# Kernel tuning notes

Measured on AMD Instinct MI355X. Metric: run time of the kernel, lower is better.

Reference implementation:

```python
import jax, jax.numpy as jnp
import numpy as np

B, M, K, N = 2, 4096, 4096, 4096

def setup_inputs() -> dict:
    key = jax.random.key(0)
    k1, k2 = jax.random.split(key)
    x = jax.random.normal(k1, (B, M, K), dtype=jnp.float32)
    y = jax.random.normal(k2, (B, N, K), dtype=jnp.float32)
    # set_activation_scale: clip = 2 * mean(|t|) when unset
    x_clip = (2.0 * jnp.abs(x).mean()).astype(jnp.float32)
    y_clip = (2.0 * jnp.abs(y).mean()).astype(jnp.float32)
    return {"x": x, "y": y, "x_clip": x_clip, "y_clip": y_clip}

def reference(x, y, x_clip, y_clip):
    # CUTLASS binary (XNOR/popcount) GEMM == sign(x) @ sign(y)^T, scaled by clips.
    # x: [B,M,K], y: [B,N,K] -> out: [B,M,N]
    out = jnp.einsum('bmk,bnk->bmn', jnp.sign(x), jnp.sign(y))
    return out * x_clip * y_clip
```

## Files before the change

### kernel.cpp

```cpp
#include <hip/hip_runtime.h>
#include <stdint.h>

#define B_ 2
#define M_ 4096
#define N_ 4096
#define K_ 4096
#define WPR 128
#define NCH 64
#define TM 128
#define TN 128
#define LDR 80

typedef int v4i  __attribute__((ext_vector_type(4)));
typedef int v16i __attribute__((ext_vector_type(16)));

__global__ __launch_bounds__(256) void pack_rows(
    const float* __restrict__ x, const float* __restrict__ y,
    uint32_t* __restrict__ px, uint32_t* __restrict__ py,
    int* __restrict__ rpx, int* __restrict__ rpy) {
    const float* in = blockIdx.y ? y : x;
    uint32_t* out   = blockIdx.y ? py : px;
    int* rp         = blockIdx.y ? rpy : rpx;
    const int wid  = (blockIdx.x * blockDim.x + threadIdx.x) >> 6;
    const int half = (threadIdx.x >> 5) & 1;
    const int l    = threadIdx.x & 31;
    const int row  = wid * 2 + half;
    const float4* src = (const float4*)(in + (size_t)row * K_);
    uint32_t r0 = 0, r1 = 0, r2 = 0, r3 = 0;
#pragma unroll 8
    for (int j = 0; j < 32; ++j) {
        float4 f = src[j * 32 + l];
        r0 = (r0 << 1) | (__float_as_uint(f.x) >> 31);
        r1 = (r1 << 1) | (__float_as_uint(f.y) >> 31);
        r2 = (r2 << 1) | (__float_as_uint(f.z) >> 31);
        r3 = (r3 << 1) | (__float_as_uint(f.w) >> 31);
    }
    ((uint4*)(out + (size_t)row * WPR))[l] = make_uint4(r0, r1, r2, r3);
    int p = __popc(r0) + __popc(r1) + __popc(r2) + __popc(r3);
#pragma unroll
    for (int off = 1; off < 32; off <<= 1) p += __shfl_xor(p, off);
    if (l == 0) rp[row] = p;
}

__global__ __launch_bounds__(256, 4) void bgemm_i8(
    const uint32_t* __restrict__ pxw, const uint32_t* __restrict__ pyw,
    const int* __restrict__ rpx, const int* __restrict__ rpy,
    float* __restrict__ out, const float* __restrict__ xclip,
    const float* __restrict__ yclip) {
    __shared__ uint8_t As[2][TM * LDR];
    __shared__ uint8_t Bs[2][TN * LDR];

    const int b    = blockIdx.z;
    const int m0   = blockIdx.x * TM;
    const int n0   = blockIdx.y * TN;
    const int t    = threadIdx.x;
    const int lane = t & 63;
    const int w    = t >> 6;
    const int wr   = w >> 1, wc = w & 1;

    const int er = t >> 1;
    const int wh = t & 1;
    const uint32_t* gA = pxw + ((size_t)(b * M_ + m0 + er)) * WPR + wh;
    const uint32_t* gB = pyw + ((size_t)(b * N_ + n0 + er)) * WPR + wh;

    v16i acc[2][2];
#pragma unroll
    for (int ti = 0; ti < 2; ++ti)
#pragma unroll
        for (int tj = 0; tj < 2; ++tj)
#pragma unroll
            for (int r = 0; r < 16; ++r) acc[ti][tj][r] = 0;

#define EXPAND_STORE(wv, base)                                              \
    {                                                                       \
        uint32_t d0 = (wv)&0x01010101u, d1 = ((wv) >> 1) & 0x01010101u;     \
        uint32_t d2 = ((wv) >> 2) & 0x01010101u, d3 = ((wv) >> 3) & 0x01010101u; \
        uint32_t d4 = ((wv) >> 4) & 0x01010101u, d5 = ((wv) >> 5) & 0x01010101u; \
        uint32_t d6 = ((wv) >> 6) & 0x01010101u, d7 = ((wv) >> 7) & 0x01010101u; \
        uint4* p_ = (uint4*)((base) + er * LDR + wh * 32);                  \
        p_[0] = make_uint4(d0, d1, d2, d3);                                 \
        p_[1] = make_uint4(d4, d5, d6, d7);                                 \
    }

    uint32_t wa = gA[0], wb = gB[0];
    EXPAND_STORE(wa, As[0]);
    EXPAND_STORE(wb, Bs[0]);
    __syncthreads();

    for (int c = 0; c < NCH; ++c) {
        const int buf = c & 1;
        if (c + 1 < NCH) {
            wa = gA[2 * (c + 1)];
            wb = gB[2 * (c + 1)];
        }
#pragma unroll
        for (int ks = 0; ks < 2; ++ks) {
            v4i af[2], bf[2];
#pragma unroll
            for (int ti = 0; ti < 2; ++ti) {
                int r = wr * 64 + ti * 32 + (lane & 31);
                af[ti] = *(const v4i*)(&As[buf][r * LDR + ks * 32 + (lane >> 5) * 16]);
            }
#pragma unroll
            for (int tj = 0; tj < 2; ++tj) {
                int r = wc * 64 + tj * 32 + (lane & 31);
                bf[tj] = *(const v4i*)(&Bs[buf][r * LDR + ks * 32 + (lane >> 5) * 16]);
            }
#pragma unroll
            for (int ti = 0; ti < 2; ++ti)
#pragma unroll
                for (int tj = 0; tj < 2; ++tj)
                    acc[ti][tj] = __builtin_amdgcn_mfma_i32_32x32x32_i8(
                        af[ti], bf[tj], acc[ti][tj], 0, 0, 0);
        }
        if (c + 1 < NCH) {
            EXPAND_STORE(wa, As[buf ^ 1]);
            EXPAND_STORE(wb, Bs[buf ^ 1]);
        }
        __syncthreads();
    }

    const float scale = xclip[0] * yclip[0];
    const int col   = lane & 31;
    const int rquad = (lane >> 5) * 4;
#pragma unroll
    for (int ti = 0; ti < 2; ++ti) {
#pragma unroll
        for (int r = 0; r < 16; ++r) {
            int rowl = (r & 3) + 8 * (r >> 2) + rquad;
            int mm = m0 + wr * 64 + ti * 32 + rowl;
            int pav = rpx[b * M_ + mm];
            float* orow = out + ((size_t)b * M_ + mm) * (size_t)N_;
#pragma unroll
            for (int tj = 0; tj < 2; ++tj) {
                int nn = n0 + wc * 64 + tj * 32 + col;
                int pbv = rpy[b * N_ + nn];
                int ci = K_ - 2 * (pav + pbv) + 4 * acc[ti][tj][r];
                orow[nn] = scale * (float)ci;
            }
        }
    }
}

extern "C" void kernel_launch(void* const* d_in, const int* in_sizes, int n_in,
                              void* d_out, int out_size, void* d_ws, size_t ws_size,
                              hipStream_t stream) {
    const float* x     = (const float*)d_in[0];
    const float* y     = (const float*)d_in[1];
    const float* xclip = (const float*)d_in[2];
    const float* yclip = (const float*)d_in[3];
    float* out = (float*)d_out;

    uint32_t* px = (uint32_t*)d_ws;
    uint32_t* py = px + (size_t)B_ * M_ * WPR;
    int* rpx = (int*)(py + (size_t)B_ * N_ * WPR);
    int* rpy = rpx + B_ * M_;

    hipLaunchKernelGGL(pack_rows, dim3(1024, 2), dim3(256), 0, stream,
                       x, y, px, py, rpx, rpy);

    dim3 grid(M_ / TM, N_ / TN, B_);
    hipLaunchKernelGGL(bgemm_i8, grid, dim3(256), 0, stream,
                       px, py, rpx, rpy, out, xclip, yclip);
}
```

Before: 440.2 us.

## Encode signs as FP4 ±1 and use scaled f8f6f4 MFMA

Each packed sign bit is expanded into an FP4 (E2M1) nibble encoding +1 or -1 instead of a 0/1 int8 byte. The GEMM then uses the MFMA 32x32x64 f8f6f4 scaled instruction in FP4 mode with unit scales, which doubles K per instruction and halves the main-loop trip count. Because ±1 values are multiplied directly, the popcount row sums and the K-2(pa+pb)+4acc correction are removed, so the pack kernel and epilogue get lighter. The risks are the correctness of the FP4 nibble layout and the fp32 accumulation, which is exact here because sums are bounded by K.

Measured after the change: 374.8 us. 1.17x faster.

```diff
diff --git a/kernel.cpp b/kernel.cpp
--- a/kernel.cpp
+++ b/kernel.cpp
@@ -6,21 +6,20 @@
 #define N_ 4096
 #define K_ 4096
 #define WPR 128
-#define NCH 64
+#define NIT 32
 #define TM 128
 #define TN 128
 #define LDR 80
 
-typedef int v4i  __attribute__((ext_vector_type(4)));
-typedef int v16i __attribute__((ext_vector_type(16)));
+typedef int v4i   __attribute__((ext_vector_type(4)));
+typedef int v8i   __attribute__((ext_vector_type(8)));
+typedef float v16f __attribute__((ext_vector_type(16)));
 
 __global__ __launch_bounds__(256) void pack_rows(
     const float* __restrict__ x, const float* __restrict__ y,
-    uint32_t* __restrict__ px, uint32_t* __restrict__ py,
-    int* __restrict__ rpx, int* __restrict__ rpy) {
+    uint32_t* __restrict__ px, uint32_t* __restrict__ py) {
     const float* in = blockIdx.y ? y : x;
     uint32_t* out   = blockIdx.y ? py : px;
-    int* rp         = blockIdx.y ? rpy : rpx;
     const int wid  = (blockIdx.x * blockDim.x + threadIdx.x) >> 6;
     const int half = (threadIdx.x >> 5) & 1;
     const int l    = threadIdx.x & 31;
@@ -36,15 +35,10 @@
         r3 = (r3 << 1) | (__float_as_uint(f.w) >> 31);
     }
     ((uint4*)(out + (size_t)row * WPR))[l] = make_uint4(r0, r1, r2, r3);
-    int p = __popc(r0) + __popc(r1) + __popc(r2) + __popc(r3);
-#pragma unroll
-    for (int off = 1; off < 32; off <<= 1) p += __shfl_xor(p, off);
-    if (l == 0) rp[row] = p;
 }
 
-__global__ __launch_bounds__(256, 4) void bgemm_i8(
+__global__ __launch_bounds__(256, 4) void bgemm_fp4(
     const uint32_t* __restrict__ pxw, const uint32_t* __restrict__ pyw,
-    const int* __restrict__ rpx, const int* __restrict__ rpy,
     float* __restrict__ out, const float* __restrict__ xclip,
     const float* __restrict__ yclip) {
     __shared__ uint8_t As[2][TM * LDR];
@@ -60,60 +54,71 @@
 
     const int er = t >> 1;
     const int wh = t & 1;
-    const uint32_t* gA = pxw + ((size_t)(b * M_ + m0 + er)) * WPR + wh;
-    const uint32_t* gB = pyw + ((size_t)(b * N_ + n0 + er)) * WPR + wh;
+    const uint32_t* gA = pxw + ((size_t)(b * M_ + m0 + er)) * WPR + 2 * wh;
+    const uint32_t* gB = pyw + ((size_t)(b * N_ + n0 + er)) * WPR + 2 * wh;
 
-    v16i acc[2][2];
+    v16f acc[2][2];
 #pragma unroll
     for (int ti = 0; ti < 2; ++ti)
 #pragma unroll
         for (int tj = 0; tj < 2; ++tj)
 #pragma unroll
-            for (int r = 0; r < 16; ++r) acc[ti][tj][r] = 0;
+            for (int r = 0; r < 16; ++r) acc[ti][tj][r] = 0.0f;
 
-#define EXPAND_STORE(wv, base)                                              \
-    {                                                                       \
-        uint32_t d0 = (wv)&0x01010101u, d1 = ((wv) >> 1) & 0x01010101u;     \
-        uint32_t d2 = ((wv) >> 2) & 0x01010101u, d3 = ((wv) >> 3) & 0x01010101u; \
-        uint32_t d4 = ((wv) >> 4) & 0x01010101u, d5 = ((wv) >> 5) & 0x01010101u; \
-        uint32_t d6 = ((wv) >> 6) & 0x01010101u, d7 = ((wv) >> 7) & 0x01010101u; \
-        uint4* p_ = (uint4*)((base) + er * LDR + wh * 32);                  \
-        p_[0] = make_uint4(d0, d1, d2, d3);                                 \
-        p_[1] = make_uint4(d4, d5, d6, d7);                                 \
+#define EXPAND_STORE(w2, base)                                               \
+    {                                                                        \
+        uint32_t _a = (w2).x, _b = (w2).y;                                   \
+        uint4* p_ = (uint4*)((base) + er * LDR + wh * 32);                   \
+        p_[0] = make_uint4(0x22222222u | ((_a & 0x11111111u) << 3),          \
+                           0x22222222u | (((_a >> 1) & 0x11111111u) << 3),   \
+                           0x22222222u | (((_a >> 2) & 0x11111111u) << 3),   \
+                           0x22222222u | (((_a >> 3) & 0x11111111u) << 3));  \
+        p_[1] = make_uint4(0x22222222u | ((_b & 0x11111111u) << 3),          \
+                           0x22222222u | (((_b >> 1) & 0x11111111u) << 3),   \
+                           0x22222222u | (((_b >> 2) & 0x11111111u) << 3),   \
+                           0x22222222u | (((_b >> 3) & 0x11111111u) << 3));  \
     }
 
-    uint32_t wa = gA[0], wb = gB[0];
+    uint2 wa = *(const uint2*)gA;
+    uint2 wb = *(const uint2*)gB;
     EXPAND_STORE(wa, As[0]);
     EXPAND_STORE(wb, Bs[0]);
     __syncthreads();
 
-    for (int c = 0; c < NCH; ++c) {
+    v8i a8[2], b8[2];
+#pragma unroll
+    for (int i = 0; i < 2; ++i)
+#pragma unroll
+        for (int j = 0; j < 8; ++j) { a8[i][j] = 0; b8[i][j] = 0; }
+
+    const int hi16 = (lane >> 5) * 16;
+    const int ar   = wr * 64 + (lane & 31);
+    const int br   = wc * 64 + (lane & 31);
+
+    for (int c = 0; c < NIT; ++c) {
         const int buf = c & 1;
-        if (c + 1 < NCH) {
-            wa = gA[2 * (c + 1)];
-            wb = gB[2 * (c + 1)];
+        if (c + 1 < NIT) {
+            wa = *(const uint2*)(gA + 4 * (c + 1));
+            wb = *(const uint2*)(gB + 4 * (c + 1));
         }
 #pragma unroll
         for (int ks = 0; ks < 2; ++ks) {
-            v4i af[2], bf[2];
 #pragma unroll
             for (int ti = 0; ti < 2; ++ti) {
-                int r = wr * 64 + ti * 32 + (lane & 31);
-                af[ti] = *(const v4i*)(&As[buf][r * LDR + ks * 32 + (lane >> 5) * 16]);
-            }
-#pragma unroll
-            for (int tj = 0; tj < 2; ++tj) {
-                int r = wc * 64 + tj * 32 + (lane & 31);
-                bf[tj] = *(const v4i*)(&Bs[buf][r * LDR + ks * 32 + (lane >> 5) * 16]);
+                *(v4i*)&a8[ti] =
+                    *(const v4i*)(&As[buf][(ar + ti * 32) * LDR + ks * 32 + hi16]);
+                *(v4i*)&b8[ti] =
+                    *(const v4i*)(&Bs[buf][(br + ti * 32) * LDR + ks * 32 + hi16]);
             }
 #pragma unroll
             for (int ti = 0; ti < 2; ++ti)
 #pragma unroll
                 for (int tj = 0; tj < 2; ++tj)
-                    acc[ti][tj] = __builtin_amdgcn_mfma_i32_32x32x32_i8(
-                        af[ti], bf[tj], acc[ti][tj], 0, 0, 0);
+                    acc[ti][tj] = __builtin_amdgcn_mfma_scale_f32_32x32x64_f8f6f4(
+                        a8[ti], b8[tj], acc[ti][tj], 4, 4,
+                        0, 0x7F7F7F7F, 0, 0x7F7F7F7F);
         }
-        if (c + 1 < NCH) {
+        if (c + 1 < NIT) {
             EXPAND_STORE(wa, As[buf ^ 1]);
             EXPAND_STORE(wb, Bs[buf ^ 1]);
         }
@@ -129,14 +134,11 @@
         for (int r = 0; r < 16; ++r) {
             int rowl = (r & 3) + 8 * (r >> 2) + rquad;
             int mm = m0 + wr * 64 + ti * 32 + rowl;
-            int pav = rpx[b * M_ + mm];
             float* orow = out + ((size_t)b * M_ + mm) * (size_t)N_;
 #pragma unroll
             for (int tj = 0; tj < 2; ++tj) {
                 int nn = n0 + wc * 64 + tj * 32 + col;
-                int pbv = rpy[b * N_ + nn];
-                int ci = K_ - 2 * (pav + pbv) + 4 * acc[ti][tj][r];
-                orow[nn] = scale * (float)ci;
+                orow[nn] = scale * acc[ti][tj][r];
             }
         }
     }
@@ -153,13 +155,11 @@
 
     uint32_t* px = (uint32_t*)d_ws;
     uint32_t* py = px + (size_t)B_ * M_ * WPR;
-    int* rpx = (int*)(py + (size_t)B_ * N_ * WPR);
-    int* rpy = rpx + B_ * M_;
 
     hipLaunchKernelGGL(pack_rows, dim3(1024, 2), dim3(256), 0, stream,
-                       x, y, px, py, rpx, rpy);
+                       x, y, px, py);
 
     dim3 grid(M_ / TM, N_ / TN, B_);
-    hipLaunchKernelGGL(bgemm_i8, grid, dim3(256), 0, stream,
-                       px, py, rpx, rpy, out, xclip, yclip);
+    hipLaunchKernelGGL(bgemm_fp4, grid, dim3(256), 0, stream,
+                       px, py, out, xclip, yclip);
 }
```
